# Kernel optimization log

Measured on AMD Instinct MI355X. Metric: run time of the kernel, lower is better.

## Reference

```python
import jax, jax.numpy as jnp
import numpy as np

# dims (match init_kwargs)
L, CH, PIX, PAT, RC, BD, OUT, B = 64, 16, 256, 64, 32, 64, 10, 256


def setup_inputs() -> dict:
    key = jax.random.key(0)
    ks = jax.random.split(key, 10)
    sd = lambda k, shape, s: jax.random.normal(k, shape, dtype=jnp.float32) * s
    # stds calibrated so each bond-contraction step has ~unit gain (quimb's
    # MPS_rand_state produces normalized states; this mirrors that stability)
    chi_first = sd(ks[0], (RC, CH), 0.70)               # (r, phys)
    chi_mid   = sd(ks[1], (L - 2, RC, RC, CH), 0.70)    # (site, l, r, phys)
    chi_last  = sd(ks[2], (RC, CH, OUT), 0.70 * 0.01)   # (l, phys, out) -- new_ind rand_strength=0.01
    psi_first = sd(ks[3], (BD, PIX), 1.0 / 32)
    psi_mid   = sd(ks[4], (L - 2, BD, BD, PIX), 1.0 / 32)
    psi_last  = sd(ks[5], (BD, PIX), 1.0 / 32)
    phi_first = sd(ks[6], (BD, PAT), 0.125)
    phi_mid   = sd(ks[7], (L - 2, BD, BD, PAT), 0.125)
    phi_last  = sd(ks[8], (BD, PAT), 0.125)
    x = jax.random.normal(ks[9], (B, PAT, PIX, CH), dtype=jnp.float32)
    return dict(x=x, chi_first=chi_first, chi_mid=chi_mid, chi_last=chi_last,
                psi_first=psi_first, psi_mid=psi_mid, psi_last=psi_last,
                phi_first=phi_first, phi_mid=phi_mid, phi_last=phi_last)


def _batched_chain(first, mid, vecs):
    # first: (bond, p); mid: (L-2, l, r, p); vecs: (L, B, p)
    v0 = jnp.einsum('rp,bp->br', first, vecs[0])
    def step(v, wu):
        W, u = wu
        return jnp.einsum('bl,lrp,bp->br', v, W, u), None
    v, _ = jax.lax.scan(step, v0, (mid, vecs[1:-1]))
    return v  # (B, bond)


def reference(x, chi_first, chi_mid, chi_last, psi_first, psi_mid, psi_last,
              phi_first, phi_mid, phi_last):
    Bn, nP, nPix, nCh = x.shape
    idx = jnp.arange(L) % nP  # site -> patch index (identity when L == n_patches)
    # per-site input vectors (contract phys legs of each MPS with data)
    vch = jnp.transpose(x.mean(axis=-2)[:, idx, :], (1, 0, 2))  # (L, B, CH)
    vpx = jnp.transpose(x.mean(axis=-1)[:, idx, :], (1, 0, 2))  # (L, B, PIX)
    # chi chain -> (B, out)
    v_chi = _batched_chain(chi_first, chi_mid, vch)
    chi_out = jnp.einsum('bl,lpo,bp->bo', v_chi, chi_last, vch[-1])
    # psi chain -> (B,)
    v_psi = _batched_chain(psi_first, psi_mid, vpx)
    psi_val = jnp.einsum('bl,lp,bp->b', v_psi, psi_last, vpx[-1])
    # phi chain: one-hot patch positions, batch-independent -> scalar
    e = jax.nn.one_hot(idx, nP, dtype=x.dtype)  # (L, PAT)
    u0 = jnp.einsum('rp,p->r', phi_first, e[0])
    def pstep(v, wu):
        W, u = wu
        return jnp.einsum('l,lrp,p->r', v, W, u), None
    u, _ = jax.lax.scan(pstep, u0, (phi_mid, e[1:-1]))
    phi_val = jnp.einsum('l,lp,p->', u, phi_last, e[-1])
    return chi_out * (psi_val * phi_val)[:, None]  # (B, out)
```

## Files before the change

kernel.cpp:

```cpp
#include <hip/hip_runtime.h>


static inline int imin(int a, int b) { return a < b ? a : b; }

typedef __attribute__((ext_vector_type(4))) float f32x4;
typedef _Float16 f16;
typedef __attribute__((ext_vector_type(8))) _Float16 f16x8;

__global__ __launch_bounds__(256) void k_reduce_x(const float* __restrict__ x,
                                                  float* __restrict__ vch,
                                                  float* __restrict__ vpx,
                                                  f16* __restrict__ vpxf,
                                                  const float* __restrict__ phi_mid,
                                                  float* __restrict__ slices) {
  if (blockIdx.x >= 16384) {
    int i = blockIdx.x - 16384;
    int t = threadIdx.x;
    #pragma unroll
    for (int k = 0; k < 16; ++k) {
      int idx = t + k * 256;
      slices[(size_t)i * 4096 + idx] = phi_mid[((size_t)i * 4096 + idx) * 64 + (i + 1)];
    }
    return;
  }
  int bp = blockIdx.x;
  int b = bp >> 6, s = bp & 63;
  int q = threadIdx.x;
  const float* row = x + ((size_t)bp << 12) + q * 16;
  float4 r0 = *(const float4*)(row);
  float4 r1 = *(const float4*)(row + 4);
  float4 r2 = *(const float4*)(row + 8);
  float4 r3 = *(const float4*)(row + 12);
  float csum = r0.x + r0.y + r0.z + r0.w + r1.x + r1.y + r1.z + r1.w
             + r2.x + r2.y + r2.z + r2.w + r3.x + r3.y + r3.z + r3.w;
  float val = csum * (1.0f / 16.0f);
  if (vpx && (s == 0 || s == 63)) vpx[((size_t)s * 256 + b) * 256 + q] = val;
  if (vpxf && s >= 1 && s <= 62) {
    size_t fa = (size_t)s * 65536
              + (((size_t)(q >> 5) * 16 + (b >> 4)) * 64 + (((q >> 3) & 3) * 16 + (b & 15))) * 8
              + (q & 7);
    vpxf[fa] = (f16)val;
  }

  __shared__ float sc[256][20];
  *(float4*)&sc[q][0]  = r0;
  *(float4*)&sc[q][4]  = r1;
  *(float4*)&sc[q][8]  = r2;
  *(float4*)&sc[q][12] = r3;
  __syncthreads();
  int c = q & 15, g = q >> 4;
  float ps = 0.f;
  #pragma unroll
  for (int k = 0; k < 16; ++k) ps += sc[g * 16 + k][c];
  __shared__ float p2[16][17];
  p2[g][c] = ps;
  __syncthreads();
  if (q < 16) {
    float s2 = 0.f;
    #pragma unroll
    for (int k = 0; k < 16; ++k) s2 += p2[k][q];
    vch[((size_t)s * 256 + b) * 16 + q] = s2 * (1.0f / 256.0f);
  }
}

__device__ __forceinline__ void psi_gemm_tile(const float* __restrict__ W,
                                              const f16* __restrict__ Afg,
                                              f16* __restrict__ Mz,
                                              int lr0, int t,
                                              unsigned char* smem) {
  typedef f16 BArr[2][2][4][64][8];
  BArr& Bf = *reinterpret_cast<BArr*>(smem);
  int lane = t & 63, w = t >> 6;
  int row = t >> 3, kg = t & 7;
  float4 sv0, sv1;

  #define LOADP(p) do {                                                      \
    const float* src = W + (size_t)(lr0 + row) * 256 + ((p) << 6) + kg * 8;  \
    sv0 = *(const float4*)src;                                               \
    sv1 = *(const float4*)(src + 4);                                         \
  } while (0)
  #define WRITEP(d) do {                                                     \
    float xs[8] = {sv0.x, sv0.y, sv0.z, sv0.w, sv1.x, sv1.y, sv1.z, sv1.w};  \
    f16x8 fv;                                                                \
    _Pragma("unroll")                                                        \
    for (int i = 0; i < 8; ++i) fv[i] = (f16)xs[i];                          \
    int ck = kg >> 2, nt = row >> 4, ln = ((kg & 3) << 4) | (row & 15);      \
    *(f16x8*)&Bf[d][ck][nt][ln][0] = fv;                                     \
  } while (0)
  #define LOADA(slot, chunk) do {                                            \
    _Pragma("unroll")                                                        \
    for (int mi = 0; mi < 2; ++mi) {                                         \
      size_t fo = ((size_t)(chunk) * 16 + (w * 2 + mi)) * 512 + (size_t)lane * 8; \
      Af[slot][mi] = *(const f16x8*)(Afg + fo);                              \
    }                                                                        \
  } while (0)

  f32x4 acc[2][4];
  #pragma unroll
  for (int i = 0; i < 2; ++i)
    #pragma unroll
    for (int j = 0; j < 4; ++j) acc[i][j] = (f32x4){0.f, 0.f, 0.f, 0.f};
  f16x8 Af[2][2];

  LOADA(0, 0);
  LOADP(0);
  WRITEP(0);
  __syncthreads();
  #pragma unroll
  for (int p = 0; p < 4; ++p) {
    if (p < 3) LOADP(p + 1);
    #pragma unroll
    for (int c = 0; c < 2; ++c) {
      const int chunk = p * 2 + c;
      const int cur = chunk & 1, nxt = (chunk + 1) & 1;
      if (chunk < 7) LOADA(nxt, chunk + 1);
      #pragma unroll
      for (int n = 0; n < 4; ++n) {
        f16x8 bf = *(const f16x8*)&Bf[p & 1][c][n][lane][0];
        #pragma unroll
        for (int mi = 0; mi < 2; ++mi) {
          acc[mi][n] = __builtin_amdgcn_mfma_f32_16x16x32_f16(Af[cur][mi], bf, acc[mi][n], 0, 0, 0);
        }
      }
    }
    if (p < 3) WRITEP((p + 1) & 1);
    __syncthreads();
  }
  #undef LOADP
  #undef WRITEP
  #undef LOADA

  int rg = lane >> 4, cidx = lane & 15;
  f16 (*T)[72] = reinterpret_cast<f16 (*)[72]>(smem);
  #pragma unroll
  for (int pass = 0; pass < 2; ++pass) {
    if ((w >> 2) == pass) {
      #pragma unroll
      for (int mi = 0; mi < 2; ++mi) {
        int rowb = (((w & 3) * 2 + mi) * 16) + rg * 4;
        #pragma unroll
        for (int n = 0; n < 4; ++n) {
          #pragma unroll
          for (int r = 0; r < 4; ++r) {
            T[rowb + r][n * 16 + cidx] = (f16)acc[mi][n][r];
          }
        }
      }
    }
    __syncthreads();
    int boff = pass * 128;
    #pragma unroll
    for (int k = 0; k < 2; ++k) {
      int f = t + k * 512;
      int b2 = f >> 3;
      int l8 = (f & 7) * 8;
      *(f16x8*)(Mz + ((size_t)(boff + b2)) * 4096 + lr0 + l8) =
          *(const f16x8*)&T[b2][l8];
    }
    __syncthreads();
  }
}

__global__ __launch_bounds__(512) void k_mega_A(const float* __restrict__ psi_mid,
                                                const f16* __restrict__ vpxf,
                                                f16* __restrict__ M,
                                                const float* __restrict__ chi_mid,
                                                const float* __restrict__ vch,
                                                float* __restrict__ Tc,
                                                const float* __restrict__ slices,
                                                const float* __restrict__ phi_first,
                                                const float* __restrict__ phi_last,
                                                float* __restrict__ phiv) {
  int bx = blockIdx.x;
  int t = threadIdx.x;
  if (bx == 0) {
    int r = t & 63, g = t >> 6;
    __shared__ float u[64];
    __shared__ float part[8][64];
    __shared__ float red[64];
    if (t < 64) u[t] = phi_first[t * 64];
    __syncthreads();
    for (int i2 = 0; i2 < 62; ++i2) {
      float sum = 0.f;
      #pragma unroll
      for (int j = 0; j < 8; ++j) {
        int l = g * 8 + j;
        sum += u[l] * slices[(size_t)i2 * 4096 + l * 64 + r];
      }
      part[g][r] = sum;
      __syncthreads();
      if (g == 0) u[r] = part[0][r] + part[1][r] + part[2][r] + part[3][r]
                       + part[4][r] + part[5][r] + part[6][r] + part[7][r];
      __syncthreads();
    }
    if (t < 64) red[t] = u[t] * phi_last[t * 64 + 63];
    __syncthreads();
    if (t == 0) {
      float s = 0.f;
      for (int l = 0; l < 64; ++l) s += red[l];
      *phiv = s;
    }
  } else if (bx <= 496) {
    int i = bx - 1;
    int z = i >> 3;
    int b0 = (i & 7) * 32;
    __shared__ float uv[32][16];
    if (t < 128) {
      int idx = t * 4;
      int b = idx >> 4, c = idx & 15;
      *(float4*)&uv[b][c] = *(const float4*)(vch + ((size_t)(z + 1) * 256 + b0 + b) * 16 + c);
    }
    __syncthreads();
    #pragma unroll
    for (int k = 0; k < 2; ++k) {
      int idx = t + k * 512;
      int r = idx >> 5, l = idx & 31;
      const float* Wp = chi_mid + ((size_t)z * 1024 + l * 32 + r) * 16;
      float4 w0 = *(const float4*)(Wp);
      float4 w1 = *(const float4*)(Wp + 4);
      float4 w2 = *(const float4*)(Wp + 8);
      float4 w3 = *(const float4*)(Wp + 12);
      for (int b = 0; b < 32; ++b) {
        const float* u = uv[b];
        float d = w0.x * u[0] + w0.y * u[1] + w0.z * u[2] + w0.w * u[3]
                + w1.x * u[4] + w1.y * u[5] + w1.z * u[6] + w1.w * u[7]
                + w2.x * u[8] + w2.y * u[9] + w2.z * u[10] + w2.w * u[11]
                + w3.x * u[12] + w3.y * u[13] + w3.z * u[14] + w3.w * u[15];
        Tc[((size_t)z * 256 + b0 + b) * 1024 + idx] = d;
      }
    }
  } else {
    int idx = bx - 497;
    int z = idx >> 6;
    int lr0 = (idx & 63) * 64;
    __shared__ __align__(16) unsigned char smem[18432];
    psi_gemm_tile(psi_mid + (size_t)z * 4096 * 256,
                  vpxf + (size_t)(z + 1) * 65536,
                  M + (size_t)z * 256 * 4096, lr0, t, smem);
  }
}

__global__ __launch_bounds__(512) void k_mega_B(const float* __restrict__ psi_mid,
                                                const f16* __restrict__ vpxf,
                                                f16* __restrict__ M,
                                                const float* __restrict__ Tc,
                                                const float* __restrict__ vpx,
                                                const float* __restrict__ vch,
                                                const float* __restrict__ psi_first,
                                                const float* __restrict__ chi_first,
                                                const float* __restrict__ chi_last,
                                                float* __restrict__ vpsi,
                                                float* __restrict__ chiout) {
  int bx = blockIdx.x;
  int t = threadIdx.x;
  if (bx < 256) {
    int b = bx;
    int r = t & 63, g = t >> 6;
    __shared__ float vsh[64];
    __shared__ float part[8][64];
    {
      const float* u0 = vpx + (size_t)b * 256;
      const float* pf = psi_first + r * 256 + g * 32;
      float s0 = 0.f;
      #pragma unroll
      for (int p = 0; p < 32; ++p) s0 += pf[p] * u0[g * 32 + p];
      part[g][r] = s0;
      __syncthreads();
      if (g == 0) {
        float sv = 0.f;
        #pragma unroll
        for (int k = 0; k < 8; ++k) sv += part[k][r];
        vsh[r] = sv;
      }
      __syncthreads();
    }
    #define QLOAD(buf, sc) do {                                                \
      const f16* Mb = M + ((size_t)(sc) * 256 + b) * 4096 + r;                 \
      _Pragma("unroll")                                                        \
      for (int j = 0; j < 8; ++j) buf[j] = (float)Mb[(size_t)(g * 8 + j) * 64]; \
    } while (0)
    #define QSTEP(buf) do {                                                    \
      float sum = 0.f;                                                         \
      _Pragma("unroll")                                                        \
      for (int j = 0; j < 8; ++j) sum += vsh[g * 8 + j] * buf[j];              \
      part[g][r] = sum;                                                        \
      __syncthreads();                                                         \
      if (g == 0) {                                                            \
        float sv = 0.f;                                                        \
        _Pragma("unroll")                                                      \
        for (int k = 0; k < 8; ++k) sv += part[k][r];                          \
        vsh[r] = sv;                                                           \
      }                                                                        \
      __syncthreads();                                                         \
    } while (0)
    float bufA[8], bufB[8];
    QLOAD(bufA, 0);
    #pragma unroll 1
    for (int sc = 0; sc < 32; sc += 2) {
      QLOAD(bufB, sc + 1);
      QSTEP(bufA);
      if (sc + 2 < 32) QLOAD(bufA, sc + 2);
      QSTEP(bufB);
    }
    #undef QLOAD
    #undef QSTEP
    if (g == 0) vpsi[b * 64 + r] = vsh[r];
  } else if (bx < 512) {
    if (t >= 64) return;
    int b = bx - 256;
    int lane = t;
    int r = lane & 31, h = lane >> 5;
    float v;
    {
      const float* u0 = vch + (size_t)b * 16;
      const float* cf = chi_first + r * 16;
      float s0 = 0.f;
      #pragma unroll
      for (int c = 0; c < 16; ++c) s0 += cf[c] * u0[c];
      v = s0;
    }
    #define CLOADX(buf, sc) do {                                               \
      const float* Mb = Tc + ((size_t)(sc) * 256 + b) * 1024 + r * 32 + h * 16; \
      *(float4*)&buf[0]  = *(const float4*)(Mb);                               \
      *(float4*)&buf[4]  = *(const float4*)(Mb + 4);                           \
      *(float4*)&buf[8]  = *(const float4*)(Mb + 8);                           \
      *(float4*)&buf[12] = *(const float4*)(Mb + 12);                          \
    } while (0)
    #define CSTEPX(buf) do {                                                   \
      float s0 = 0.f, s1 = 0.f;                                                \
      _Pragma("unroll")                                                        \
      for (int j = 0; j < 8; ++j) {                                            \
        s0 += __shfl(v, h * 16 + 2 * j)     * buf[2 * j];                      \
        s1 += __shfl(v, h * 16 + 2 * j + 1) * buf[2 * j + 1];                  \
      }                                                                        \
      float sum = s0 + s1;                                                     \
      sum += __shfl_xor(sum, 32);                                              \
      v = sum;                                                                 \
    } while (0)
    {
      float mjA[16], mjB[16];
      CLOADX(mjA, 0);
      #pragma unroll 1
      for (int sc = 0; sc < 62; sc += 2) {
        CLOADX(mjB, sc + 1);
        CSTEPX(mjA);
        if (sc + 2 < 62) CLOADX(mjA, sc + 2);
        CSTEPX(mjB);
      }
    }
    #undef CLOADX
    #undef CSTEPX
    const float* u63 = vch + ((size_t)63 * 256 + b) * 16;
    float uc[16];
    #pragma unroll
    for (int c = 0; c < 16; ++c) uc[c] = u63[c];
    for (int o = 0; o < 10; ++o) {
      const float* cl = chi_last + r * 16 * 10 + o;
      float wv = 0.f;
      #pragma unroll
      for (int c = 0; c < 16; ++c) wv += cl[c * 10] * uc[c];
      float p = v * wv;
      #pragma unroll
      for (int m = 32; m > 0; m >>= 1) p += __shfl_xor(p, m);
      if (lane == 0) chiout[b * 10 + o] = p * 0.5f;
    }
  } else {
    int idx = bx - 512;
    int z = 32 + (idx >> 6);
    int lr0 = (idx & 63) * 64;
    __shared__ __align__(16) unsigned char smem[18432];
    psi_gemm_tile(psi_mid + (size_t)z * 4096 * 256,
                  vpxf + (size_t)(z + 1) * 65536,
                  M + (size_t)z * 256 * 4096, lr0, t, smem);
  }
}

__global__ __launch_bounds__(64) void k_chain_tail(const f16* __restrict__ M,
                                                   const float* __restrict__ vpx,
                                                   const float* __restrict__ psi_last,
                                                   const float* __restrict__ chiout,
                                                   const float* __restrict__ phiv,
                                                   const float* __restrict__ vpsi,
                                                   float* __restrict__ out) {
  int b = blockIdx.x;
  int lane = threadIdx.x;
  float v = vpsi[b * 64 + lane];
  #define MLOAD(buf, sc) do {                                                \
    const f16* Mb = M + ((size_t)(32 + (sc)) * 256 + b) * 4096 + lane;       \
    _Pragma("unroll")                                                        \
    for (int l = 0; l < 64; ++l) buf[l] = (float)Mb[(size_t)l * 64];         \
  } while (0)
  #define MSTEP(buf) do {                                                    \
    float s0 = 0.f, s1 = 0.f, s2 = 0.f, s3 = 0.f;                            \
    _Pragma("unroll")                                                        \
    for (int l = 0; l < 16; ++l) {                                           \
      s0 += __shfl(v, 4 * l + 0) * buf[4 * l + 0];                           \
      s1 += __shfl(v, 4 * l + 1) * buf[4 * l + 1];                           \
      s2 += __shfl(v, 4 * l + 2) * buf[4 * l + 2];                           \
      s3 += __shfl(v, 4 * l + 3) * buf[4 * l + 3];                           \
    }                                                                        \
    v = (s0 + s1) + (s2 + s3);                                               \
  } while (0)
  {
    float mvA[64], mvB[64];
    MLOAD(mvA, 0);
    #pragma unroll 1
    for (int sc = 0; sc < 30; sc += 2) {
      MLOAD(mvB, sc + 1);
      MSTEP(mvA);
      if (sc + 2 < 30) MLOAD(mvA, sc + 2);
      MSTEP(mvB);
    }
  }
  #undef MLOAD
  #undef MSTEP
  float acc_p = 0.f;
  #pragma unroll
  for (int pp = 0; pp < 4; ++pp) {
    int p = pp * 64 + lane;
    float pl[64];
    #pragma unroll
    for (int l = 0; l < 64; ++l) pl[l] = psi_last[l * 256 + p];
    float s0 = 0.f, s1 = 0.f, s2 = 0.f, s3 = 0.f;
    #pragma unroll
    for (int l = 0; l < 16; ++l) {
      s0 += __shfl(v, 4 * l + 0) * pl[4 * l + 0];
      s1 += __shfl(v, 4 * l + 1) * pl[4 * l + 1];
      s2 += __shfl(v, 4 * l + 2) * pl[4 * l + 2];
      s3 += __shfl(v, 4 * l + 3) * pl[4 * l + 3];
    }
    float wv = (s0 + s1) + (s2 + s3);
    acc_p += wv * vpx[((size_t)63 * 256 + b) * 256 + p];
  }
  #pragma unroll
  for (int m = 32; m > 0; m >>= 1) acc_p += __shfl_xor(acc_p, m);
  if (lane < 10) out[b * 10 + lane] = chiout[b * 10 + lane] * acc_p * phiv[0];
}

__global__ __launch_bounds__(512) void k_psi_gemm(const float* __restrict__ psi_mid,
                                                  const f16* __restrict__ vpxf,
                                                  f16* __restrict__ M, int s0) {
  int z = blockIdx.z;
  int s = s0 + z;
  int lr0 = blockIdx.x * 64;
  __shared__ __align__(16) unsigned char smem[18432];
  psi_gemm_tile(psi_mid + (size_t)s * 4096 * 256,
                vpxf + (size_t)(s + 1) * 65536,
                M + (size_t)z * 256 * 4096, lr0, threadIdx.x, smem);
}

__global__ __launch_bounds__(256) void k_psi_chain(const f16* __restrict__ M,
                                                   const float* __restrict__ vpx,
                                                   const float* __restrict__ psi_first,
                                                   const float* __restrict__ psi_last,
                                                   float* __restrict__ vpsi,
                                                   float* __restrict__ psiv,
                                                   int nS, int isFirst, int isLast) {
  int b = blockIdx.x;
  int t = threadIdx.x;
  int r = t & 63, g = t >> 6;
  __shared__ float v[64];
  __shared__ float part[4][64];
  __shared__ float red[256];
  if (isFirst) {
    const float* u0 = vpx + (size_t)b * 256;
    float s0 = 0.f;
    for (int p = g * 64; p < g * 64 + 64; ++p) s0 += psi_first[r * 256 + p] * u0[p];
    part[g][r] = s0;
    __syncthreads();
    if (g == 0) v[r] = part[0][r] + part[1][r] + part[2][r] + part[3][r];
    __syncthreads();
  } else {
    if (g == 0) v[r] = vpsi[b * 64 + r];
    __syncthreads();
  }
  for (int sc = 0; sc < nS; ++sc) {
    const f16* Mb = M + ((size_t)sc * 256 + b) * 4096;
    float sum = 0.f;
    #pragma unroll
    for (int j = 0; j < 16; ++j) {
      int l = g * 16 + j;
      sum += v[l] * (float)Mb[l * 64 + r];
    }
    part[g][r] = sum;
    __syncthreads();
    if (g == 0) v[r] = part[0][r] + part[1][r] + part[2][r] + part[3][r];
    __syncthreads();
  }
  if (isLast) {
    float qv = 0.f;
    for (int l = 0; l < 64; ++l) qv += v[l] * psi_last[l * 256 + t];
    red[t] = qv * vpx[((size_t)63 * 256 + b) * 256 + t];
    __syncthreads();
    for (int off = 128; off > 0; off >>= 1) {
      if (t < off) red[t] += red[t + off];
      __syncthreads();
    }
    if (t == 0) psiv[b] = red[0];
  } else {
    if (g == 0) vpsi[b * 64 + r] = v[r];
  }
}

__device__ __forceinline__ void phi_chain_body(const float* __restrict__ slices,
                                               const float* __restrict__ phi_first,
                                               const float* __restrict__ phi_last,
                                               float* __restrict__ phiv) {
  int t = threadIdx.x;
  int r = t & 63, g = t >> 6;
  __shared__ float u[64];
  __shared__ float part[4][64];
  __shared__ float red[64];
  if (t < 64) u[t] = phi_first[t * 64];
  __syncthreads();
  for (int i = 0; i < 62; ++i) {
    float sum = 0.f;
    #pragma unroll
    for (int j = 0; j < 16; ++j) {
      int l = g * 16 + j;
      sum += u[l] * slices[(size_t)i * 4096 + l * 64 + r];
    }
    part[g][r] = sum;
    __syncthreads();
    if (g == 0) u[r] = part[0][r] + part[1][r] + part[2][r] + part[3][r];
    __syncthreads();
  }
  if (t < 64) red[t] = u[t] * phi_last[t * 64 + 63];
  __syncthreads();
  if (t == 0) {
    float s = 0.f;
    for (int l = 0; l < 64; ++l) s += red[l];
    *phiv = s;
  }
}

__global__ __launch_bounds__(256) void k_phi_chain(const float* __restrict__ slices,
                                                   const float* __restrict__ phi_first,
                                                   const float* __restrict__ phi_last,
                                                   float* __restrict__ phiv) {
  phi_chain_body(slices, phi_first, phi_last, phiv);
}

__global__ __launch_bounds__(256) void k_chi_gemm(const float* __restrict__ chi_mid,
                                                  const float* __restrict__ vch,
                                                  float* __restrict__ Tc, int s0,
                                                  int phiBlock,
                                                  const float* __restrict__ slices,
                                                  const float* __restrict__ phi_first,
                                                  const float* __restrict__ phi_last,
                                                  float* __restrict__ phiv) {
  if ((int)blockIdx.x == phiBlock) {
    if (blockIdx.y == 0) phi_chain_body(slices, phi_first, phi_last, phiv);
    return;
  }
  int z = blockIdx.x;
  int s = s0 + z;
  int b0 = blockIdx.y * 32;
  int t = threadIdx.x;
  __shared__ float uv[32][16];
  if (t < 128) {
    int idx = t * 4;
    int b = idx >> 4, c = idx & 15;
    *(float4*)&uv[b][c] = *(const float4*)(vch + ((size_t)(s + 1) * 256 + b0 + b) * 16 + c);
  }
  __syncthreads();
  #pragma unroll
  for (int k = 0; k < 4; ++k) {
    int idx = t + k * 256;
    int r = idx >> 5, l = idx & 31;
    const float* Wp = chi_mid + ((size_t)s * 1024 + l * 32 + r) * 16;
    float4 w0 = *(const float4*)(Wp);
    float4 w1 = *(const float4*)(Wp + 4);
    float4 w2 = *(const float4*)(Wp + 8);
    float4 w3 = *(const float4*)(Wp + 12);
    for (int b = 0; b < 32; ++b) {
      const float* u = uv[b];
      float d = w0.x * u[0] + w0.y * u[1] + w0.z * u[2] + w0.w * u[3]
              + w1.x * u[4] + w1.y * u[5] + w1.z * u[6] + w1.w * u[7]
              + w2.x * u[8] + w2.y * u[9] + w2.z * u[10] + w2.w * u[11]
              + w3.x * u[12] + w3.y * u[13] + w3.z * u[14] + w3.w * u[15];
      Tc[((size_t)z * 256 + b0 + b) * 1024 + idx] = d;
    }
  }
}

__global__ __launch_bounds__(64) void k_chi_chain(const float* __restrict__ Tc,
                                                  const float* __restrict__ chi_first,
                                                  const float* __restrict__ chi_last,
                                                  const float* __restrict__ vch,
                                                  const float* __restrict__ psiv,
                                                  const float* __restrict__ phiv,
                                                  float* __restrict__ vchi,
                                                  float* __restrict__ out,
                                                  int nS, int isFirst, int isLast) {
  int b = blockIdx.x;
  int lane = threadIdx.x;
  int r = lane & 31, h = lane >> 5;
  __shared__ float v[32];
  if (isFirst) {
    if (h == 0) {
      const float* u0 = vch + (size_t)b * 16;
      const float* cf = chi_first + r * 16;
      float s0 = 0.f;
      #pragma unroll
      for (int c = 0; c < 16; ++c) s0 += cf[c] * u0[c];
      v[r] = s0;
    }
  } else {
    if (h == 0) v[r] = vchi[b * 32 + r];
  }
  __syncthreads();
  for (int sc = 0; sc < nS; ++sc) {
    const float* Mb = Tc + ((size_t)sc * 256 + b) * 1024 + r * 32 + h * 16;
    float4 m0 = *(const float4*)(Mb);
    float4 m1 = *(const float4*)(Mb + 4);
    float4 m2 = *(const float4*)(Mb + 8);
    float4 m3 = *(const float4*)(Mb + 12);
    const float* vv = &v[h * 16];
    float sum = m0.x * vv[0] + m0.y * vv[1] + m0.z * vv[2] + m0.w * vv[3]
              + m1.x * vv[4] + m1.y * vv[5] + m1.z * vv[6] + m1.w * vv[7]
              + m2.x * vv[8] + m2.y * vv[9] + m2.z * vv[10] + m2.w * vv[11]
              + m3.x * vv[12] + m3.y * vv[13] + m3.z * vv[14] + m3.w * vv[15];
    sum += __shfl_xor(sum, 32);
    __syncthreads();
    if (h == 0) v[r] = sum;
    __syncthreads();
  }
  if (isLast) {
    const float* u63 = vch + ((size_t)63 * 256 + b) * 16;
    float uc[16];
    #pragma unroll
    for (int c = 0; c < 16; ++c) uc[c] = u63[c];
    float scale = 0.5f * psiv[b] * phiv[0];
    for (int o = 0; o < 10; ++o) {
      const float* cl = chi_last + r * 16 * 10 + o;
      float w = 0.f;
      #pragma unroll
      for (int c = 0; c < 16; ++c) w += cl[c * 10] * uc[c];
      float p = v[r] * w;
      #pragma unroll
      for (int m = 32; m > 0; m >>= 1) p += __shfl_xor(p, m);
      if (lane == 0) out[b * 10 + o] = p * scale;
    }
  } else {
    if (h == 0) vchi[b * 32 + r] = v[r];
  }
}

__global__ __launch_bounds__(256) void k_chi_fused(const float* __restrict__ chi_first,
                                                   const float* __restrict__ chi_mid,
                                                   const float* __restrict__ chi_last,
                                                   const float* __restrict__ vch,
                                                   const float* __restrict__ psiv,
                                                   const float* __restrict__ phiv,
                                                   float* __restrict__ out) {
  int t = threadIdx.x;
  int bl = t >> 6, lg = (t >> 5) & 1, r = t & 31;
  int b = blockIdx.x * 4 + bl;
  __shared__ float v[4][32];
  __shared__ float part[4][2][32];
  if (lg == 0) {
    const float* u0 = vch + (size_t)b * 16;
    float s0 = 0.f;
    #pragma unroll
    for (int c = 0; c < 16; ++c) s0 += chi_first[r * 16 + c] * u0[c];
    v[bl][r] = s0;
  }
  __syncthreads();
  for (int s = 0; s < 62; ++s) {
    const float* u = vch + ((size_t)(s + 1) * 256 + b) * 16;
    float uc[16];
    #pragma unroll
    for (int c = 0; c < 16; ++c) uc[c] = u[c];
    const float* W = chi_mid + (size_t)s * 32 * 32 * 16;
    float sum = 0.f;
    #pragma unroll
    for (int j = 0; j < 16; ++j) {
      int l = lg * 16 + j;
      const float* Wl = W + ((size_t)l * 32 + r) * 16;
      float tt = 0.f;
      #pragma unroll
      for (int c = 0; c < 16; ++c) tt += Wl[c] * uc[c];
      sum += v[bl][l] * tt;
    }
    part[bl][lg][r] = sum;
    __syncthreads();
    if (lg == 0) v[bl][r] = part[bl][0][r] + part[bl][1][r];
    __syncthreads();
  }
  const float* u63 = vch + ((size_t)63 * 256 + b) * 16;
  float uc[16];
  #pragma unroll
  for (int c = 0; c < 16; ++c) uc[c] = u63[c];
  if (r < 10) {
    float acc = 0.f;
    #pragma unroll
    for (int j = 0; j < 16; ++j) {
      int l = lg * 16 + j;
      const float* cl = chi_last + (size_t)l * 16 * 10;
      float tt = 0.f;
      #pragma unroll
      for (int c = 0; c < 16; ++c) tt += cl[c * 10 + r] * uc[c];
      acc += v[bl][l] * tt;
    }
    part[bl][lg][r] = acc;
  }
  __syncthreads();
  if (lg == 0 && r < 10)
    out[b * 10 + r] = (part[bl][0][r] + part[bl][1][r]) * psiv[b] * phiv[0];
}

__global__ __launch_bounds__(256) void k_psi_direct(const float* __restrict__ x,
                                                    const float* __restrict__ psi_mid,
                                                    const float* __restrict__ psi_first,
                                                    const float* __restrict__ psi_last,
                                                    float* __restrict__ psiv) {
  int b = blockIdx.x;
  int t = threadIdx.x;
  int r = t & 63, g = t >> 6;
  __shared__ float u[256];
  __shared__ float v[64];
  __shared__ float part[4][64];
  __shared__ float red[256];
  const float* xb = x + ((size_t)b << 18);
  {
    const float* rw = xb + (size_t)0 * 4096 + t * 16;
    float sm = 0.f;
    #pragma unroll
    for (int c = 0; c < 16; ++c) sm += rw[c];
    u[t] = sm * (1.0f / 16.0f);
  }
  __syncthreads();
  {
    float s0 = 0.f;
    for (int p = g * 64; p < g * 64 + 64; ++p) s0 += psi_first[r * 256 + p] * u[p];
    part[g][r] = s0;
    __syncthreads();
    if (g == 0) v[r] = part[0][r] + part[1][r] + part[2][r] + part[3][r];
  }
  __syncthreads();
  for (int s = 0; s < 62; ++s) {
    __syncthreads();
    {
      const float* rw = xb + (size_t)(s + 1) * 4096 + t * 16;
      float sm = 0.f;
      #pragma unroll
      for (int c = 0; c < 16; ++c) sm += rw[c];
      u[t] = sm * (1.0f / 16.0f);
    }
    __syncthreads();
    const float* W = psi_mid + (size_t)s * 4096 * 256;
    float sum = 0.f;
    for (int l = 0; l < 64; ++l) {
      const float* Wl = W + ((size_t)(l * 64 + r)) * 256 + g * 64;
      float tt = 0.f;
      #pragma unroll 8
      for (int k = 0; k < 64; ++k) tt += Wl[k] * u[g * 64 + k];
      sum += v[l] * tt;
    }
    part[g][r] = sum;
    __syncthreads();
    if (g == 0) v[r] = part[0][r] + part[1][r] + part[2][r] + part[3][r];
    __syncthreads();
  }
  __syncthreads();
  {
    const float* rw = xb + (size_t)63 * 4096 + t * 16;
    float sm = 0.f;
    #pragma unroll
    for (int c = 0; c < 16; ++c) sm += rw[c];
    u[t] = sm * (1.0f / 16.0f);
  }
  __syncthreads();
  float qv = 0.f;
  for (int l = 0; l < 64; ++l) qv += v[l] * psi_last[l * 256 + t];
  red[t] = qv * u[t];
  __syncthreads();
  for (int off = 128; off > 0; off >>= 1) {
    if (t < off) red[t] += red[t + off];
    __syncthreads();
  }
  if (t == 0) psiv[b] = red[0];
}

extern "C" void kernel_launch(void* const* d_in, const int* in_sizes, int n_in,
                              void* d_out, int out_size, void* d_ws, size_t ws_size,
                              hipStream_t stream) {
  const float* x         = (const float*)d_in[0];
  const float* chi_first = (const float*)d_in[1];
  const float* chi_mid   = (const float*)d_in[2];
  const float* chi_last  = (const float*)d_in[3];
  const float* psi_first = (const float*)d_in[4];
  const float* psi_mid   = (const float*)d_in[5];
  const float* psi_last  = (const float*)d_in[6];
  const float* phi_first = (const float*)d_in[7];
  const float* phi_mid   = (const float*)d_in[8];
  const float* phi_last  = (const float*)d_in[9];
  float* out = (float*)d_out;
  float* ws  = (float*)d_ws;

  size_t wsf = ws_size / 4;
  size_t off = 0;
  float* vch    = ws + off; off += (size_t)64 * 256 * 16;
  float* psiv   = ws + off; off += 256;
  float* chiout = ws + off; off += 2560;
  float* phisl  = ws + off; off += (size_t)62 * 64 * 64;
  float* phiv   = ws + off; off += 16;
  float* vpsi   = ws + off; off += (size_t)64 * 256;
  float* vchi   = ws + off; off += (size_t)32 * 256;
  float* vpx    = ws + off; off += (size_t)64 * 256 * 256;
  f16* vpxf = (f16*)(ws + off); off += (size_t)64 * 65536 / 2;
  f16* Mbuf = (f16*)(ws + off);
  size_t needMh  = (size_t)62 * 256 * 4096;
  float* Tcbuf = (float*)(Mbuf + needMh);
  size_t needTc = (size_t)62 * 256 * 1024;
  size_t bytes_needed = off * 4 + needMh * 2 + needTc * 4;

  if (ws_size >= bytes_needed) {
    k_reduce_x<<<16384 + 62, 256, 0, stream>>>(x, vch, vpx, vpxf,
                                               phi_mid, phisl);
    k_mega_A<<<497 + 2048, 512, 0, stream>>>(psi_mid, vpxf, Mbuf,
                                             chi_mid, vch, Tcbuf,
                                             phisl, phi_first, phi_last, phiv);
    k_mega_B<<<512 + 1920, 512, 0, stream>>>(psi_mid, vpxf, Mbuf,
                                             Tcbuf, vpx, vch, psi_first,
                                             chi_first, chi_last, vpsi, chiout);
    k_chain_tail<<<256, 64, 0, stream>>>(Mbuf, vpx, psi_last, chiout, phiv,
                                         vpsi, out);
  } else {
    size_t avail_b = (ws_size > off * 4) ? ws_size - off * 4 : 0;
    int C = (int)(avail_b / ((size_t)256 * 4096 * 2));
    if (C > 62) C = 62;
    int Cc = (int)(avail_b / ((size_t)256 * 1024 * 4));
    if (Cc > 62) Cc = 62;
    if (C >= 1) {
      k_reduce_x<<<16384 + 62, 256, 0, stream>>>(x, vch, vpx, vpxf,
                                                 phi_mid, phisl);
      int done = 0;
      while (done < 62) {
        int c = imin(C, 62 - done);
        k_psi_gemm<<<dim3(64, 1, c), 512, 0, stream>>>(psi_mid, vpxf, Mbuf, done);
        k_psi_chain<<<256, 256, 0, stream>>>(Mbuf, vpx, psi_first, psi_last,
                                             vpsi, psiv, c, (done == 0) ? 1 : 0,
                                             (done + c == 62) ? 1 : 0);
        done += c;
      }
      done = 0;
      while (done < 62) {
        int c = imin(Cc, 62 - done);
        int phiBlk = (done == 0) ? c : -1;
        int gx = (done == 0) ? (c + 1) : c;
        k_chi_gemm<<<dim3(gx, 8), 256, 0, stream>>>(chi_mid, vch, (float*)Mbuf, done, phiBlk,
                                                    phisl, phi_first, phi_last, phiv);
        k_chi_chain<<<256, 64, 0, stream>>>((float*)Mbuf, chi_first, chi_last, vch,
                                            psiv, phiv, vchi, out, c,
                                            (done == 0) ? 1 : 0,
                                            (done + c == 62) ? 1 : 0);
        done += c;
      }
    } else {
      k_reduce_x<<<16384 + 62, 256, 0, stream>>>(x, vch, nullptr, nullptr,
                                                 phi_mid, phisl);
      k_psi_direct<<<256, 256, 0, stream>>>(x, psi_mid, psi_first, psi_last, psiv);
      k_phi_chain<<<1, 256, 0, stream>>>(phisl, phi_first, phi_last, phiv);
      k_chi_fused<<<64, 256, 0, stream>>>(chi_first, chi_mid, chi_last, vch, psiv, phiv, out);
    }
  }
}
```

Before: 253.7 us.

## Deepen psi GEMM prefetch pipeline and rebalance site split across mega kernels

The psi GEMM tile now keeps two register sets for W prefetches, so each panel is loaded two stages before its shared-memory write rather than one, giving more load latency hiding. Separately, the boundary between sites handled in k_mega_A and k_mega_B moves from 32 to 36. Mega_A gains GEMM tiles, mega_B's chain walks 36 steps, and the tail chain shrinks to 26 steps. The extra live registers may hurt occupancy, and the rebalance shifts work between concurrent roles in each kernel.

```diff
diff --git a/kernel.cpp b/kernel.cpp
--- a/kernel.cpp
+++ b/kernel.cpp
@@ -72,15 +72,28 @@
   BArr& Bf = *reinterpret_cast<BArr*>(smem);
   int lane = t & 63, w = t >> 6;
   int row = t >> 3, kg = t & 7;
-  float4 sv0, sv1;
-
-  #define LOADP(p) do {                                                      \
+  float4 svA0, svA1, svB0, svB1;
+
+  #define LOADPA(p) do {                                                     \
     const float* src = W + (size_t)(lr0 + row) * 256 + ((p) << 6) + kg * 8;  \
-    sv0 = *(const float4*)src;                                               \
-    sv1 = *(const float4*)(src + 4);                                         \
+    svA0 = *(const float4*)src;                                              \
+    svA1 = *(const float4*)(src + 4);                                        \
   } while (0)
-  #define WRITEP(d) do {                                                     \
-    float xs[8] = {sv0.x, sv0.y, sv0.z, sv0.w, sv1.x, sv1.y, sv1.z, sv1.w};  \
+  #define LOADPB(p) do {                                                     \
+    const float* src = W + (size_t)(lr0 + row) * 256 + ((p) << 6) + kg * 8;  \
+    svB0 = *(const float4*)src;                                              \
+    svB1 = *(const float4*)(src + 4);                                        \
+  } while (0)
+  #define WRITEPA(d) do {                                                    \
+    float xs[8] = {svA0.x, svA0.y, svA0.z, svA0.w, svA1.x, svA1.y, svA1.z, svA1.w}; \
+    f16x8 fv;                                                                \
+    _Pragma("unroll")                                                        \
+    for (int i = 0; i < 8; ++i) fv[i] = (f16)xs[i];                          \
+    int ck = kg >> 2, nt = row >> 4, ln = ((kg & 3) << 4) | (row & 15);      \
+    *(f16x8*)&Bf[d][ck][nt][ln][0] = fv;                                     \
+  } while (0)
+  #define WRITEPB(d) do {                                                    \
+    float xs[8] = {svB0.x, svB0.y, svB0.z, svB0.w, svB1.x, svB1.y, svB1.z, svB1.w}; \
     f16x8 fv;                                                                \
     _Pragma("unroll")                                                        \
     for (int i = 0; i < 8; ++i) fv[i] = (f16)xs[i];                          \
@@ -94,6 +107,22 @@
       Af[slot][mi] = *(const f16x8*)(Afg + fo);                              \
     }                                                                        \
   } while (0)
+  #define COMPUTE(p) do {                                                    \
+    _Pragma("unroll")                                                        \
+    for (int c = 0; c < 2; ++c) {                                            \
+      const int chunk = (p) * 2 + c;                                         \
+      const int cur = chunk & 1, nxt = (chunk + 1) & 1;                      \
+      if (chunk < 7) LOADA(nxt, chunk + 1);                                  \
+      _Pragma("unroll")                                                      \
+      for (int n = 0; n < 4; ++n) {                                          \
+        f16x8 bf = *(const f16x8*)&Bf[(p) & 1][c][n][lane][0];               \
+        _Pragma("unroll")                                                    \
+        for (int mi = 0; mi < 2; ++mi) {                                     \
+          acc[mi][n] = __builtin_amdgcn_mfma_f32_16x16x32_f16(Af[cur][mi], bf, acc[mi][n], 0, 0, 0); \
+        }                                                                    \
+      }                                                                      \
+    }                                                                        \
+  } while (0)
 
   f32x4 acc[2][4];
   #pragma unroll
@@ -103,32 +132,29 @@
   f16x8 Af[2][2];
 
   LOADA(0, 0);
-  LOADP(0);
-  WRITEP(0);
-  __syncthreads();
-  #pragma unroll
-  for (int p = 0; p < 4; ++p) {
-    if (p < 3) LOADP(p + 1);
-    #pragma unroll
-    for (int c = 0; c < 2; ++c) {
-      const int chunk = p * 2 + c;
-      const int cur = chunk & 1, nxt = (chunk + 1) & 1;
-      if (chunk < 7) LOADA(nxt, chunk + 1);
-      #pragma unroll
-      for (int n = 0; n < 4; ++n) {
-        f16x8 bf = *(const f16x8*)&Bf[p & 1][c][n][lane][0];
-        #pragma unroll
-        for (int mi = 0; mi < 2; ++mi) {
-          acc[mi][n] = __builtin_amdgcn_mfma_f32_16x16x32_f16(Af[cur][mi], bf, acc[mi][n], 0, 0, 0);
-        }
-      }
-    }
-    if (p < 3) WRITEP((p + 1) & 1);
-    __syncthreads();
-  }
-  #undef LOADP
-  #undef WRITEP
+  LOADPA(0);
+  LOADPB(1);
+  WRITEPA(0);
+  __syncthreads();
+  LOADPA(2);
+  COMPUTE(0);
+  WRITEPB(1);
+  __syncthreads();
+  LOADPB(3);
+  COMPUTE(1);
+  WRITEPA(0);
+  __syncthreads();
+  COMPUTE(2);
+  WRITEPB(1);
+  __syncthreads();
+  COMPUTE(3);
+  __syncthreads();
+  #undef LOADPA
+  #undef LOADPB
+  #undef WRITEPA
+  #undef WRITEPB
   #undef LOADA
+  #undef COMPUTE
 
   int rg = lane >> 4, cidx = lane & 15;
   f16 (*T)[72] = reinterpret_cast<f16 (*)[72]>(smem);
@@ -296,10 +322,10 @@
     float bufA[8], bufB[8];
     QLOAD(bufA, 0);
     #pragma unroll 1
-    for (int sc = 0; sc < 32; sc += 2) {
+    for (int sc = 0; sc < 36; sc += 2) {
       QLOAD(bufB, sc + 1);
       QSTEP(bufA);
-      if (sc + 2 < 32) QLOAD(bufA, sc + 2);
+      if (sc + 2 < 36) QLOAD(bufA, sc + 2);
       QSTEP(bufB);
     }
     #undef QLOAD
@@ -366,7 +392,7 @@
     }
   } else {
     int idx = bx - 512;
-    int z = 32 + (idx >> 6);
+    int z = 36 + (idx >> 6);
     int lr0 = (idx & 63) * 64;
     __shared__ __align__(16) unsigned char smem[18432];
     psi_gemm_tile(psi_mid + (size_t)z * 4096 * 256,
@@ -386,7 +412,7 @@
   int lane = threadIdx.x;
   float v = vpsi[b * 64 + lane];
   #define MLOAD(buf, sc) do {                                                \
-    const f16* Mb = M + ((size_t)(32 + (sc)) * 256 + b) * 4096 + lane;       \
+    const f16* Mb = M + ((size_t)(36 + (sc)) * 256 + b) * 4096 + lane;       \
     _Pragma("unroll")                                                        \
     for (int l = 0; l < 64; ++l) buf[l] = (float)Mb[(size_t)l * 64];         \
   } while (0)
@@ -405,10 +431,10 @@
     float mvA[64], mvB[64];
     MLOAD(mvA, 0);
     #pragma unroll 1
-    for (int sc = 0; sc < 30; sc += 2) {
+    for (int sc = 0; sc < 26; sc += 2) {
       MLOAD(mvB, sc + 1);
       MSTEP(mvA);
-      if (sc + 2 < 30) MLOAD(mvA, sc + 2);
+      if (sc + 2 < 26) MLOAD(mvA, sc + 2);
       MSTEP(mvB);
     }
   }
@@ -819,10 +845,10 @@
   if (ws_size >= bytes_needed) {
     k_reduce_x<<<16384 + 62, 256, 0, stream>>>(x, vch, vpx, vpxf,
                                                phi_mid, phisl);
-    k_mega_A<<<497 + 2048, 512, 0, stream>>>(psi_mid, vpxf, Mbuf,
+    k_mega_A<<<497 + 2304, 512, 0, stream>>>(psi_mid, vpxf, Mbuf,
                                              chi_mid, vch, Tcbuf,
                                              phisl, phi_first, phi_last, phiv);
-    k_mega_B<<<512 + 1920, 512, 0, stream>>>(psi_mid, vpxf, Mbuf,
+    k_mega_B<<<512 + 1664, 512, 0, stream>>>(psi_mid, vpxf, Mbuf,
                                              Tcbuf, vpx, vch, psi_first,
                                              chi_first, chi_last, vpsi, chiout);
     k_chain_tail<<<256, 64, 0, stream>>>(Mbuf, vpx, psi_last, chiout, phiv,
```

New measurement: 248.4 us (median of 2 runs). -2.1%, faster.
